# Optimization experiments

Hardware: AMD Instinct MI355X
Metric: run time of the kernel (lower is better)

Reference implementation:

```python
import jax, jax.numpy as jnp
import numpy as np

B, S, D, H, E = 2, 512, 768, 12, 8
FF = 4 * D
HD = D // H


def setup_inputs() -> dict:
    key = jax.random.key(0)
    ks = jax.random.split(key, 12)
    s = 0.02
    return {
        "x": jax.random.normal(ks[0], (B, S, D), jnp.float32),
        "ln1_g": jnp.ones((D,), jnp.float32),
        "ln1_b": jnp.zeros((D,), jnp.float32),
        "ln2_g": jnp.ones((D,), jnp.float32),
        "ln2_b": jnp.zeros((D,), jnp.float32),
        "in_proj_w": jax.random.normal(ks[1], (3 * D, D), jnp.float32) * s,
        "in_proj_b": jax.random.normal(ks[2], (3 * D,), jnp.float32) * s,
        "out_proj_w": jax.random.normal(ks[3], (D, D), jnp.float32) * s,
        "out_proj_b": jax.random.normal(ks[4], (D,), jnp.float32) * s,
        "router_w": jax.random.normal(ks[5], (E, D), jnp.float32) * s,
        "router_b": jax.random.normal(ks[6], (E,), jnp.float32) * s,
        "w1": jax.random.normal(ks[7], (E, D, FF), jnp.float32) * s,
        "b1": jax.random.normal(ks[8], (E, FF), jnp.float32) * s,
        "w2": jax.random.normal(ks[9], (E, FF, D), jnp.float32) * s,
        "b2": jax.random.normal(ks[10], (E, D), jnp.float32) * s,
    }


def _layernorm(x, g, b, eps=1e-5):
    mu = x.mean(-1, keepdims=True)
    var = ((x - mu) ** 2).mean(-1, keepdims=True)
    return (x - mu) * jax.lax.rsqrt(var + eps) * g + b


def _forward(x, ln1_g, ln1_b, ln2_g, ln2_b, in_proj_w, in_proj_b,
             out_proj_w, out_proj_b, router_w, router_b, w1, b1, w2, b2):
    # --- self-attention sublayer (pre-norm per torch module ordering) ---
    h = _layernorm(x, ln1_g, ln1_b)
    qkv = h @ in_proj_w.T + in_proj_b                     # [B,S,3D]
    q, k, v = jnp.split(qkv, 3, axis=-1)
    to_heads = lambda t: t.reshape(B, S, H, HD).transpose(0, 2, 1, 3)  # [B,H,S,hd]
    q, k, v = to_heads(q), to_heads(k), to_heads(v)
    scores = jnp.einsum('bhqd,bhkd->bhqk', q, k) / np.float32(np.sqrt(HD))
    attn = jax.nn.softmax(scores, axis=-1)
    o = jnp.einsum('bhqk,bhkd->bhqd', attn, v).transpose(0, 2, 1, 3).reshape(B, S, D)
    o = o @ out_proj_w.T + out_proj_b
    x = x + o
    # --- MoE sublayer: top-2 routing, renormalized gates ---
    h2 = _layernorm(x, ln2_g, ln2_b)
    t = h2.reshape(-1, D)                                  # [T,D]
    logits = t @ router_w.T + router_b                     # [T,E]
    probs = jax.nn.softmax(logits, axis=-1)
    top_v, top_i = jax.lax.top_k(probs, 2)                 # [T,2]
    top_v = top_v / top_v.sum(-1, keepdims=True)
    # per-(token, expert) combine weight (0 if expert not in token's top-2)
    comb = jnp.sum(jax.nn.one_hot(top_i, E, dtype=probs.dtype) * top_v[..., None], axis=1)  # [T,E]
    # dense grouped-FFN: every token through every expert, zero-weighted combine
    hid = jax.nn.gelu(jnp.einsum('td,edf->tef', t, w1) + b1, approximate=False)  # exact GELU as torch
    y = jnp.einsum('tef,efd->ted', hid, w2) + b2           # [T,E,D]
    moe = jnp.einsum('te,ted->td', comb, y).reshape(B, S, D)
    return x + moe


def reference(x, ln1_g, ln1_b, ln2_g, ln2_b, in_proj_w, in_proj_b,
              out_proj_w, out_proj_b, router_w, router_b, w1, b1, w2, b2):
    return _forward(x, ln1_g, ln1_b, ln2_g, ln2_b, in_proj_w, in_proj_b,
                    out_proj_w, out_proj_b, router_w, router_b, w1, b1, w2, b2)
```

## Files before the change

kernel.cpp:

```cpp
#include <hip/hip_runtime.h>
#include <hip/hip_bf16.h>

#define BATCH 2
#define SEQ 512
#define DIM 768
#define HEADS 12
#define NEXP 8
#define FFDIM 3072
#define HDIM 64
#define NTOK (BATCH*SEQ)
#define NENT (2*NTOK)

typedef __hip_bfloat16 bf16;
typedef __attribute__((ext_vector_type(8))) short s8v;
typedef __attribute__((ext_vector_type(4))) float f4v;

typedef __attribute__((address_space(1))) const unsigned char gas_u8;
typedef __attribute__((address_space(3))) unsigned char las_u8;
__device__ __forceinline__ void gload16(const void* g, void* l) {
    __builtin_amdgcn_global_load_lds((gas_u8*)g, (las_u8*)l, 16, 0, 0);
}

__global__ __launch_bounds__(256) void ln_kernel(const float* __restrict__ x,
                                                 const float* __restrict__ g,
                                                 const float* __restrict__ b,
                                                 float* __restrict__ outf,
                                                 bf16* __restrict__ outb) {
    int t = blockIdx.x;
    const float* xr = x + (long)t * DIM;
    int tid = threadIdx.x;
    float v0 = xr[tid], v1 = xr[tid + 256], v2 = xr[tid + 512];
    float s = v0 + v1 + v2;
    __shared__ float red[4];
    #pragma unroll
    for (int o = 32; o; o >>= 1) s += __shfl_xor(s, o);
    if ((tid & 63) == 0) red[tid >> 6] = s;
    __syncthreads();
    s = red[0] + red[1] + red[2] + red[3];
    float mu = s * (1.f / DIM);
    float d0 = v0 - mu, d1 = v1 - mu, d2 = v2 - mu;
    float q = d0*d0 + d1*d1 + d2*d2;
    __shared__ float red2[4];
    #pragma unroll
    for (int o = 32; o; o >>= 1) q += __shfl_xor(q, o);
    if ((tid & 63) == 0) red2[tid >> 6] = q;
    __syncthreads();
    q = red2[0] + red2[1] + red2[2] + red2[3];
    float rstd = rsqrtf(q * (1.f / DIM) + 1e-5f);
    float o0 = d0 * rstd * g[tid]       + b[tid];
    float o1 = d1 * rstd * g[tid + 256] + b[tid + 256];
    float o2 = d2 * rstd * g[tid + 512] + b[tid + 512];
    if (outf) {
        float* of = outf + (long)t * DIM;
        of[tid] = o0; of[tid + 256] = o1; of[tid + 512] = o2;
    }
    if (outb) {
        bf16* ob = outb + (long)t * DIM;
        ob[tid] = __float2bfloat16(o0);
        ob[tid + 256] = __float2bfloat16(o1);
        ob[tid + 512] = __float2bfloat16(o2);
    }
}

template<int WM, int WN, bool GROUPED, bool GELU, int OUTMODE>
__global__ __launch_bounds__(256) void mfma_gemm(
    const bf16* __restrict__ A, const bf16* __restrict__ B,
    const float* __restrict__ bias, const float* __restrict__ resid,
    void* __restrict__ Cv,
    int M, int N, int K, int lda, int ldb, int ldc,
    int zdiv, int ksplit,
    long a_hi, long a_lo, long b_hi, long b_lo, long c_hi, long c_lo,
    long bias_stride, const int* __restrict__ grp_off, float alpha)
{
    constexpr int BM = 32 * WM, BN = 32 * WN;
    constexpr int ACH = BM * 4;
    constexpr int BCH = BN * 4;

    int z = blockIdx.z;
    int ze = z / ksplit, ks = z % ksplit;
    int kper = K / ksplit;
    long aoff, boff, coff;
    int m_count = M;
    if (GROUPED) {
        int m0 = grp_off[ze], m1 = grp_off[ze + 1];
        m_count = m1 - m0;
        if ((int)blockIdx.y * BM >= m_count) return;
        aoff = (long)m0 * lda;
        coff = (long)m0 * ldc;
        boff = (long)ze * b_hi;
    } else {
        int zh = ze / zdiv, zl = ze % zdiv;
        aoff = zh * a_hi + zl * a_lo;
        boff = zh * b_hi + zl * b_lo;
        coff = zh * c_hi + zl * c_lo;
    }
    const short* Ag = (const short*)(A + aoff);
    const short* Bg = (const short*)(B + boff);
    const float* biasp = bias ? bias + (long)ze * bias_stride : nullptr;
    float* Cf = (float*)Cv + coff;
    bf16*  Cb = (bf16*)Cv + coff;

    __shared__ short As[BM * 32];
    __shared__ short Bs[BN * 32];

    int tid = threadIdx.x;
    int wv = tid >> 6, ln = tid & 63;
    int wr = wv >> 1, wc = wv & 1;
    int fr = ln & 15, fq = ln >> 4;
    int bm = blockIdx.y * BM, bn = blockIdx.x * BN;

    f4v acc[WM][WN] = {};

    for (int k0 = ks * kper; k0 < (ks + 1) * kper; k0 += 32) {
        #pragma unroll
        for (int is = 0; is < ACH / 256; ++is) {
            int c = is * 256 + wv * 64 + ln;
            int m = c >> 2, kq = c & 3;
            gload16(Ag + (long)(bm + m) * lda + k0 + kq * 8,
                    &As[(is * 256 + wv * 64) * 8]);
        }
        if constexpr (ACH % 256) {
            if (tid < ACH % 256) {
                int c = (ACH / 256) * 256 + tid;
                int m = c >> 2, kq = c & 3;
                gload16(Ag + (long)(bm + m) * lda + k0 + kq * 8,
                        &As[((ACH / 256) * 256 + wv * 64) * 8]);
            }
        }
        #pragma unroll
        for (int is = 0; is < BCH / 256; ++is) {
            int c = is * 256 + wv * 64 + ln;
            int m = c >> 2, kq = c & 3;
            gload16(Bg + (long)(bn + m) * ldb + k0 + kq * 8,
                    &Bs[(is * 256 + wv * 64) * 8]);
        }
        if constexpr (BCH % 256) {
            if (tid < BCH % 256) {
                int c = (BCH / 256) * 256 + tid;
                int m = c >> 2, kq = c & 3;
                gload16(Bg + (long)(bn + m) * ldb + k0 + kq * 8,
                        &Bs[((BCH / 256) * 256 + wv * 64) * 8]);
            }
        }
        __syncthreads();
        s8v av[WM], bv[WN];
        #pragma unroll
        for (int i = 0; i < WM; ++i)
            av[i] = *(const s8v*)&As[(wr * (WM * 16) + i * 16 + fr) * 32 + fq * 8];
        #pragma unroll
        for (int j = 0; j < WN; ++j)
            bv[j] = *(const s8v*)&Bs[(wc * (WN * 16) + j * 16 + fr) * 32 + fq * 8];
        #pragma unroll
        for (int i = 0; i < WM; ++i)
            #pragma unroll
            for (int j = 0; j < WN; ++j)
                acc[i][j] = __builtin_amdgcn_mfma_f32_16x16x32_bf16(av[i], bv[j], acc[i][j], 0, 0, 0);
        __syncthreads();
    }

    #pragma unroll
    for (int i = 0; i < WM; ++i) {
        #pragma unroll
        for (int r = 0; r < 4; ++r) {
            int row = bm + wr * (WM * 16) + i * 16 + fq * 4 + r;
            if (GROUPED && row >= m_count) continue;
            #pragma unroll
            for (int j = 0; j < WN; ++j) {
                int col = bn + wc * (WN * 16) + j * 16 + fr;
                if (col < N) {
                    float v = acc[i][j][r] * alpha;
                    if (OUTMODE == 2) {
                        atomicAdd(&Cf[(long)row * ldc + col], v);
                    } else {
                        if (biasp) v += biasp[col];
                        if (GELU) v = 0.5f * v * (1.f + erff(v * 0.70710678118654752f));
                        if (resid) v += resid[(long)row * ldc + col];
                        if (OUTMODE == 1) Cb[(long)row * ldc + col] = __float2bfloat16(v);
                        else              Cf[(long)row * ldc + col] = v;
                    }
                }
            }
        }
    }
}

template<int XT, int YCAP, int KS, bool GELU, int OUTMODE>
__global__ __launch_bounds__(256) void moe_gemm(
    const bf16* __restrict__ A, const bf16* __restrict__ B,
    const float* __restrict__ bias, void* __restrict__ Cv,
    int lda, int ldb, int ldc, int Ktot, long b_hi, long bias_stride,
    const int* __restrict__ grp_off, int N)
{
    int bid = blockIdx.x;
    int e = bid & 7;
    int r = bid >> 3;
    int xt = r % XT; r /= XT;
    int yt = r % YCAP;
    int ks = r / YCAP;
    int m0 = grp_off[e], m1 = grp_off[e + 1];
    int m_count = m1 - m0;
    int bm = yt * 128;
    if (bm >= m_count) return;
    int bn = xt * 64;
    int kper = Ktot / KS;

    const short* Ag = (const short*)A + (long)m0 * lda;
    const short* Bg = (const short*)(B + (long)e * b_hi);
    const float* biasp = bias ? bias + (long)e * bias_stride : nullptr;
    float* Cf = (float*)Cv + (long)m0 * ldc;
    bf16*  Cb = (bf16*)Cv + (long)m0 * ldc;

    __shared__ short As[128 * 32];
    __shared__ short Bs[64 * 32];

    int tid = threadIdx.x;
    int wv = tid >> 6, ln = tid & 63;
    int wr = wv >> 1, wc = wv & 1;
    int fr = ln & 15, fq = ln >> 4;

    f4v acc[4][2] = {};

    for (int k0 = ks * kper; k0 < (ks + 1) * kper; k0 += 32) {
        #pragma unroll
        for (int is = 0; is < 2; ++is) {
            int c = is * 256 + wv * 64 + ln;
            int m = c >> 2, kq = c & 3;
            gload16(Ag + (long)(bm + m) * lda + k0 + kq * 8,
                    &As[(is * 256 + wv * 64) * 8]);
        }
        {
            int c = wv * 64 + ln;
            int n = c >> 2, kq = c & 3;
            gload16(Bg + (long)(bn + n) * ldb + k0 + kq * 8,
                    &Bs[(wv * 64) * 8]);
        }
        __syncthreads();
        s8v av[4], bv[2];
        #pragma unroll
        for (int i = 0; i < 4; ++i)
            av[i] = *(const s8v*)&As[(wr * 64 + i * 16 + fr) * 32 + fq * 8];
        #pragma unroll
        for (int j = 0; j < 2; ++j)
            bv[j] = *(const s8v*)&Bs[(wc * 32 + j * 16 + fr) * 32 + fq * 8];
        #pragma unroll
        for (int i = 0; i < 4; ++i)
            #pragma unroll
            for (int j = 0; j < 2; ++j)
                acc[i][j] = __builtin_amdgcn_mfma_f32_16x16x32_bf16(av[i], bv[j], acc[i][j], 0, 0, 0);
        __syncthreads();
    }

    #pragma unroll
    for (int i = 0; i < 4; ++i) {
        #pragma unroll
        for (int rr = 0; rr < 4; ++rr) {
            int row = bm + wr * 64 + i * 16 + fq * 4 + rr;
            if (row >= m_count) continue;
            #pragma unroll
            for (int j = 0; j < 2; ++j) {
                int col = bn + wc * 32 + j * 16 + fr;
                float v = acc[i][j][rr];
                if (OUTMODE == 2) {
                    atomicAdd(&Cf[(long)row * ldc + col], v);
                } else {
                    if (biasp) v += biasp[col];
                    if (GELU) v = 0.5f * v * (1.f + erff(v * 0.70710678118654752f));
                    Cb[(long)row * ldc + col] = __float2bfloat16(v);
                }
            }
        }
    }
}

__global__ __launch_bounds__(256) void softmax512(const float* __restrict__ s,
                                                  bf16* __restrict__ attn) {
    long row = blockIdx.x;
    const float* p = s + row * 512;
    int tid = threadIdx.x;
    float a = p[tid], b = p[tid + 256];
    float m = fmaxf(a, b);
    __shared__ float red[4], red2[4];
    #pragma unroll
    for (int o = 32; o; o >>= 1) m = fmaxf(m, __shfl_xor(m, o));
    if ((tid & 63) == 0) red[tid >> 6] = m;
    __syncthreads();
    m = fmaxf(fmaxf(red[0], red[1]), fmaxf(red[2], red[3]));
    float e0 = expf(a - m), e1 = expf(b - m);
    float ssum = e0 + e1;
    #pragma unroll
    for (int o = 32; o; o >>= 1) ssum += __shfl_xor(ssum, o);
    if ((tid & 63) == 0) red2[tid >> 6] = ssum;
    __syncthreads();
    ssum = red2[0] + red2[1] + red2[2] + red2[3];
    float inv = 1.f / ssum;
    bf16* ar = attn + row * 512;
    ar[tid]       = __float2bfloat16(e0 * inv);
    ar[tid + 256] = __float2bfloat16(e1 * inv);
}

__global__ __launch_bounds__(256) void vt_kernel(const bf16* __restrict__ qkvb,
                                                 bf16* __restrict__ vt) {
    int st = blockIdx.x;
    int z = blockIdx.y;
    int b = z / HEADS, h = z % HEADS;
    __shared__ short tile[64][65];
    int t = threadIdx.x;
    int d = t & 63, s0 = t >> 6;
    const short* q = (const short*)qkvb;
    #pragma unroll
    for (int i = 0; i < 16; ++i) {
        int s = st * 64 + s0 + i * 4;
        tile[s0 + i * 4][d] = q[(long)(b * SEQ + s) * 2304 + 2 * DIM + h * HDIM + d];
    }
    __syncthreads();
    short* o = (short*)vt;
    #pragma unroll
    for (int i = 0; i < 16; ++i) {
        int d2 = (t >> 6) + i * 4;
        o[(long)(z * 64 + d2) * 512 + st * 64 + (t & 63)] = tile[t & 63][d2];
    }
}

__global__ __launch_bounds__(256) void wtrans_kernel(const float* __restrict__ in,
                                                     bf16* __restrict__ out,
                                                     int R, int C) {
    int z = blockIdx.z;
    long ibase = (long)z * R * C;
    int rt = blockIdx.y * 64, ct = blockIdx.x * 64;
    __shared__ float tile[64][65];
    int t = threadIdx.x;
    int c = t & 63, r0 = t >> 6;
    #pragma unroll
    for (int i = 0; i < 16; ++i)
        tile[r0 + i * 4][c] = in[ibase + (long)(rt + r0 + i * 4) * C + ct + c];
    __syncthreads();
    #pragma unroll
    for (int i = 0; i < 16; ++i) {
        int cc = r0 + i * 4;
        out[ibase + (long)(ct + cc) * R + rt + c] = __float2bfloat16(tile[c][cc]);
    }
}

__global__ __launch_bounds__(256) void cvt_kernel(const float* __restrict__ in,
                                                  bf16* __restrict__ out, long n) {
    long i = ((long)blockIdx.x * 256 + threadIdx.x) * 4;
    if (i >= n) return;
    float4 v = *(const float4*)(in + i);
    out[i]     = __float2bfloat16(v.x);
    out[i + 1] = __float2bfloat16(v.y);
    out[i + 2] = __float2bfloat16(v.z);
    out[i + 3] = __float2bfloat16(v.w);
}

__global__ __launch_bounds__(64) void router_kernel(const float* __restrict__ t2,
                                                    const float* __restrict__ rw,
                                                    const float* __restrict__ rb,
                                                    int* __restrict__ e_sel,
                                                    float* __restrict__ w_sel) {
    int t = blockIdx.x;
    int lane = threadIdx.x;
    const float* tr = t2 + (long)t * DIM;
    float tv[12];
    #pragma unroll
    for (int i = 0; i < 12; ++i) tv[i] = tr[lane + 64 * i];
    float logits[NEXP];
    #pragma unroll
    for (int e = 0; e < NEXP; ++e) {
        const float* wr = rw + (long)e * DIM;
        float s = 0.f;
        #pragma unroll
        for (int i = 0; i < 12; ++i) s += tv[i] * wr[lane + 64 * i];
        #pragma unroll
        for (int o = 32; o; o >>= 1) s += __shfl_xor(s, o);
        logits[e] = s + rb[e];
    }
    if (lane == 0) {
        int e0 = -1, e1 = -1;
        float l0 = -1e30f, l1 = -1e30f;
        #pragma unroll
        for (int e = 0; e < NEXP; ++e) {
            float l = logits[e];
            if (l > l0) { l1 = l0; e1 = e0; l0 = l; e0 = e; }
            else if (l > l1) { l1 = l; e1 = e; }
        }
        float p1 = expf(l1 - l0);
        float inv = 1.f / (1.f + p1);
        e_sel[t * 2] = e0;  e_sel[t * 2 + 1] = e1;
        w_sel[t * 2] = inv; w_sel[t * 2 + 1] = p1 * inv;
    }
}

__global__ __launch_bounds__(1024) void build_lists(const int* __restrict__ e_sel,
                                                    int* __restrict__ entry_tok,
                                                    int* __restrict__ ent_exp,
                                                    int* __restrict__ pos,
                                                    int* __restrict__ grp_off) {
    __shared__ int cnt[NEXP];
    __shared__ int off[NEXP + 1];
    __shared__ int cur[NEXP];
    int tid = threadIdx.x;
    if (tid < NEXP) cnt[tid] = 0;
    __syncthreads();
    for (int i = tid; i < NENT; i += 1024) atomicAdd(&cnt[e_sel[i]], 1);
    __syncthreads();
    if (tid == 0) {
        off[0] = 0;
        for (int e = 0; e < NEXP; ++e) off[e + 1] = off[e] + cnt[e];
        for (int e = 0; e < NEXP; ++e) cur[e] = off[e];
    }
    __syncthreads();
    for (int i = tid; i < NENT; i += 1024) {
        int e = e_sel[i];
        int p = atomicAdd(&cur[e], 1);
        entry_tok[p] = i >> 1;
        ent_exp[p] = e;
        pos[i] = p;
    }
    if (tid < NEXP + 1) grp_off[tid] = off[tid];
}

__global__ __launch_bounds__(256) void gather_kernel(const bf16* __restrict__ t2b,
                                                     const int* __restrict__ entry_tok,
                                                     bf16* __restrict__ t2g) {
    long i = (long)blockIdx.x * 256 + threadIdx.x;
    if (i >= (long)NENT * 192) return;
    int p = (int)(i / 192), q = (int)(i % 192);
    ((uint2*)t2g)[(long)p * 192 + q] = ((const uint2*)t2b)[(long)entry_tok[p] * 192 + q];
}

__global__ __launch_bounds__(256) void prefill_x1(const float* __restrict__ x,
                                                  const float* __restrict__ out_b,
                                                  float* __restrict__ x1) {
    long i = ((long)blockIdx.x * 256 + threadIdx.x) * 4;
    if (i >= (long)NTOK * DIM) return;
    int d = (int)(i % DIM);
    float4 v = *(const float4*)(x + i);
    v.x += out_b[d]; v.y += out_b[d + 1]; v.z += out_b[d + 2]; v.w += out_b[d + 3];
    *(float4*)(x1 + i) = v;
}

__global__ __launch_bounds__(256) void prefill_ybuf(const float* __restrict__ b2,
                                                    const int* __restrict__ ent_exp,
                                                    float* __restrict__ ybuf) {
    long i = ((long)blockIdx.x * 256 + threadIdx.x) * 4;
    if (i >= (long)NENT * DIM) return;
    int p = (int)(i / DIM), d = (int)(i % DIM);
    *(float4*)(ybuf + i) = *(const float4*)(b2 + (long)ent_exp[p] * DIM + d);
}

__global__ __launch_bounds__(256) void combine_kernel(const float* __restrict__ x1,
                                                      const float* __restrict__ ybuf,
                                                      const int* __restrict__ pos,
                                                      const float* __restrict__ wsel,
                                                      float* __restrict__ out) {
    long i = (long)blockIdx.x * 256 + threadIdx.x;
    if (i >= (long)NTOK * DIM) return;
    int t = (int)(i / DIM), d = (int)(i % DIM);
    float v = x1[i];
    v += wsel[t * 2]     * ybuf[(long)pos[t * 2]     * DIM + d];
    v += wsel[t * 2 + 1] * ybuf[(long)pos[t * 2 + 1] * DIM + d];
    out[i] = v;
}

extern "C" void kernel_launch(void* const* d_in, const int* in_sizes, int n_in,
                              void* d_out, int out_size, void* d_ws, size_t ws_size,
                              hipStream_t stream) {
    const float* x        = (const float*)d_in[0];
    const float* ln1_g    = (const float*)d_in[1];
    const float* ln1_b    = (const float*)d_in[2];
    const float* ln2_g    = (const float*)d_in[3];
    const float* ln2_b    = (const float*)d_in[4];
    const float* in_w     = (const float*)d_in[5];
    const float* in_b     = (const float*)d_in[6];
    const float* out_w    = (const float*)d_in[7];
    const float* out_b    = (const float*)d_in[8];
    const float* router_w = (const float*)d_in[9];
    const float* router_b = (const float*)d_in[10];
    const float* w1       = (const float*)d_in[11];
    const float* b1       = (const float*)d_in[12];
    const float* w2       = (const float*)d_in[13];
    const float* b2       = (const float*)d_in[14];
    float* out = (float*)d_out;

    const long TD = (long)NTOK * DIM;
    char* p = (char*)d_ws;
    size_t off = 0;
    auto alloc = [&](size_t bytes) -> void* {
        void* r = p + off; off += (bytes + 255) & ~(size_t)255; return r;
    };
    bf16*  h_b    = (bf16*)alloc(TD * 2);
    bf16*  in_wb  = (bf16*)alloc(2304L * 768 * 2);
    bf16*  qkv_b  = (bf16*)alloc(1024L * 2304 * 2);
    bf16*  out_wb = (bf16*)alloc(768L * 768 * 2);
    bf16*  vt_b   = (bf16*)alloc((24L * 64 + 64) * 512 * 2);
    bf16*  oat_b  = (bf16*)alloc(TD * 2);
    float* x1     = (float*)alloc(TD * 4);
    float* t2     = (float*)alloc(TD * 4);
    bf16*  t2b    = (bf16*)alloc(TD * 2);
    bf16*  t2g    = (bf16*)alloc((2048L + 256) * 768 * 2);
    bf16*  w1t    = (bf16*)alloc(8L * 3072 * 768 * 2);
    bf16*  w2t    = (bf16*)alloc(8L * 768 * 3072 * 2);
    bf16*  hid    = (bf16*)alloc((2048L + 256) * 3072 * 2);
    float* ybuf   = (float*)alloc(2048L * 768 * 4);
    int*   e_sel     = (int*)alloc(NENT * 4);
    float* w_sel     = (float*)alloc(NENT * 4);
    int*   entry_tok = (int*)alloc(NENT * 4);
    int*   ent_exp   = (int*)alloc(NENT * 4);
    int*   pos       = (int*)alloc(NENT * 4);
    int*   grp_off   = (int*)alloc(64);
    float* scores = (float*)w1t;
    bf16*  attn   = (bf16*)((char*)w1t + 24L * 512 * 512 * 4);

    ln_kernel<<<NTOK, 256, 0, stream>>>(x, ln1_g, ln1_b, nullptr, h_b);
    cvt_kernel<<<1728, 256, 0, stream>>>(in_w, in_wb, 2304L * 768);
    cvt_kernel<<<576, 256, 0, stream>>>(out_w, out_wb, 768L * 768);
    mfma_gemm<2, 2, false, false, 1><<<dim3(36, 16, 1), 256, 0, stream>>>(
        h_b, in_wb, in_b, nullptr, qkv_b,
        NTOK, 3 * DIM, DIM, DIM, DIM, 3 * DIM,
        1, 1, 0, 0, 0, 0, 0, 0, 0, nullptr, 1.f);
    mfma_gemm<2, 4, false, false, 0><<<dim3(4, 8, 24), 256, 0, stream>>>(
        qkv_b, qkv_b + DIM, nullptr, nullptr, scores,
        SEQ, SEQ, HDIM, 3 * DIM, 3 * DIM, SEQ,
        HEADS, 1, (long)SEQ * 3 * DIM, HDIM, (long)SEQ * 3 * DIM, HDIM,
        (long)HEADS * SEQ * SEQ, (long)SEQ * SEQ,
        0, nullptr, 0.125f);
    softmax512<<<24 * SEQ, 256, 0, stream>>>(scores, attn);
    vt_kernel<<<dim3(8, 24), 256, 0, stream>>>(qkv_b, vt_b);
    mfma_gemm<1, 2, false, false, 1><<<dim3(1, 16, 24), 256, 0, stream>>>(
        attn, vt_b, nullptr, nullptr, oat_b,
        SEQ, HDIM, SEQ, SEQ, SEQ, DIM,
        HEADS, 1, (long)HEADS * SEQ * SEQ, (long)SEQ * SEQ,
        (long)HEADS * HDIM * SEQ, (long)HDIM * SEQ,
        (long)SEQ * DIM, HDIM,
        0, nullptr, 1.f);
    prefill_x1<<<768, 256, 0, stream>>>(x, out_b, x1);
    mfma_gemm<2, 2, false, false, 2><<<dim3(12, 16, 2), 256, 0, stream>>>(
        oat_b, out_wb, nullptr, nullptr, x1,
        NTOK, DIM, DIM, DIM, DIM, DIM,
        1, 2, 0, 0, 0, 0, 0, 0, 0, nullptr, 1.f);
    ln_kernel<<<NTOK, 256, 0, stream>>>(x1, ln2_g, ln2_b, t2, t2b);
    router_kernel<<<NTOK, 64, 0, stream>>>(t2, router_w, router_b, e_sel, w_sel);
    build_lists<<<1, 1024, 0, stream>>>(e_sel, entry_tok, ent_exp, pos, grp_off);
    gather_kernel<<<1536, 256, 0, stream>>>(t2b, entry_tok, t2g);
    wtrans_kernel<<<dim3(48, 12, 8), 256, 0, stream>>>(w1, w1t, DIM, FFDIM);
    moe_gemm<48, 16, 1, true, 1><<<8 * 48 * 16, 256, 0, stream>>>(
        t2g, w1t, b1, hid,
        DIM, DIM, FFDIM, DIM, (long)FFDIM * DIM, FFDIM, grp_off, FFDIM);
    wtrans_kernel<<<dim3(12, 48, 8), 256, 0, stream>>>(w2, w2t, FFDIM, DIM);
    prefill_ybuf<<<1536, 256, 0, stream>>>(b2, ent_exp, ybuf);
    moe_gemm<12, 16, 4, false, 2><<<8 * 12 * 16 * 4, 256, 0, stream>>>(
        hid, w2t, nullptr, ybuf,
        FFDIM, FFDIM, DIM, FFDIM, (long)DIM * FFDIM, 0, grp_off, DIM);
    combine_kernel<<<3072, 256, 0, stream>>>(x1, ybuf, pos, w_sel, out);
}
```

Before: 213.9 us.

## Double-buffer grouped GEMM LDS tiles with BK=64 and XOR swizzle

The grouped MoE GEMM kernel now stages A and B tiles into two LDS buffers and prefetches the next K-slice while MFMAs run on the current one. The K step per stage grows from 32 to 64, and the 16-byte chunks are XOR-swizzled by row to cut LDS bank conflicts on fragment reads. This removes one barrier per iteration and hides global load latency. In exchange LDS use per block rises fourfold, which may lower occupancy, and it requires kper to be a multiple of 64.

```diff
diff --git a/kernel.cpp b/kernel.cpp
--- a/kernel.cpp
+++ b/kernel.cpp
@@ -210,8 +210,8 @@
     float* Cf = (float*)Cv + (long)m0 * ldc;
     bf16*  Cb = (bf16*)Cv + (long)m0 * ldc;
 
-    __shared__ short As[128 * 32];
-    __shared__ short Bs[64 * 32];
+    __shared__ short As[2][128 * 64];
+    __shared__ short Bs[2][64 * 64];
 
     int tid = threadIdx.x;
     int wv = tid >> 6, ln = tid & 63;
@@ -220,34 +220,54 @@
 
     f4v acc[4][2] = {};
 
-    for (int k0 = ks * kper; k0 < (ks + 1) * kper; k0 += 32) {
+    auto stage = [&](int buf, int k0) {
+        #pragma unroll
+        for (int is = 0; is < 4; ++is) {
+            int c = is * 256 + wv * 64 + ln;
+            int m = c >> 3, q = c & 7;
+            int qg = q ^ (m & 7);
+            gload16(Ag + (long)(bm + m) * lda + k0 + qg * 8,
+                    &As[buf][(is * 256 + wv * 64) * 8]);
+        }
         #pragma unroll
         for (int is = 0; is < 2; ++is) {
             int c = is * 256 + wv * 64 + ln;
-            int m = c >> 2, kq = c & 3;
-            gload16(Ag + (long)(bm + m) * lda + k0 + kq * 8,
-                    &As[(is * 256 + wv * 64) * 8]);
-        }
-        {
-            int c = wv * 64 + ln;
-            int n = c >> 2, kq = c & 3;
-            gload16(Bg + (long)(bn + n) * ldb + k0 + kq * 8,
-                    &Bs[(wv * 64) * 8]);
+            int n = c >> 3, q = c & 7;
+            int qg = q ^ (n & 7);
+            gload16(Bg + (long)(bn + n) * ldb + k0 + qg * 8,
+                    &Bs[buf][(is * 256 + wv * 64) * 8]);
+        }
+    };
+
+    int kbeg = ks * kper;
+    int nit = kper / 64;
+    stage(0, kbeg);
+    __syncthreads();
+    int cur = 0;
+    for (int it = 0; it < nit; ++it) {
+        if (it + 1 < nit) stage(cur ^ 1, kbeg + (it + 1) * 64);
+        #pragma unroll
+        for (int ksub = 0; ksub < 2; ++ksub) {
+            s8v av[4], bv[2];
+            int qg = ksub * 4 + fq;
+            #pragma unroll
+            for (int i = 0; i < 4; ++i) {
+                int row = wr * 64 + i * 16 + fr;
+                av[i] = *(const s8v*)&As[cur][row * 64 + (qg ^ (row & 7)) * 8];
+            }
+            #pragma unroll
+            for (int j = 0; j < 2; ++j) {
+                int row = wc * 32 + j * 16 + fr;
+                bv[j] = *(const s8v*)&Bs[cur][row * 64 + (qg ^ (row & 7)) * 8];
+            }
+            #pragma unroll
+            for (int i = 0; i < 4; ++i)
+                #pragma unroll
+                for (int j = 0; j < 2; ++j)
+                    acc[i][j] = __builtin_amdgcn_mfma_f32_16x16x32_bf16(av[i], bv[j], acc[i][j], 0, 0, 0);
         }
         __syncthreads();
-        s8v av[4], bv[2];
-        #pragma unroll
-        for (int i = 0; i < 4; ++i)
-            av[i] = *(const s8v*)&As[(wr * 64 + i * 16 + fr) * 32 + fq * 8];
-        #pragma unroll
-        for (int j = 0; j < 2; ++j)
-            bv[j] = *(const s8v*)&Bs[(wc * 32 + j * 16 + fr) * 32 + fq * 8];
-        #pragma unroll
-        for (int i = 0; i < 4; ++i)
-            #pragma unroll
-            for (int j = 0; j < 2; ++j)
-                acc[i][j] = __builtin_amdgcn_mfma_f32_16x16x32_bf16(av[i], bv[j], acc[i][j], 0, 0, 0);
-        __syncthreads();
+        cur ^= 1;
     }
 
     #pragma unroll
```

New measurement: 210.5 us. About the same (-1.6%).
